# Kernel tuning notes

Measured on AMD Instinct MI355X. Metric: run time of the kernel, lower is better.

Reference implementation:

```python
import jax, jax.numpy as jnp
import numpy as np

D = 4096       # hidden_size
H = 32         # n_heads (tp_size=1)
DN = 128       # qk_nope_head_dim
DR = 64        # qk_rope_head_dim
DV = 128       # v_head_dim
QL = 1536      # q_lora_rank
KL = 512       # kv_lora_rank
S = 2048       # seqlen, start_pos = 0
EPS = 1e-6
SCALE = (DN + DR) ** -0.5  # softmax_scale (no yarn mscale: seqlen <= original_seq_len)
THETA = 10000.0


def _freqs(seqlen, dim, base=THETA):
    # precompute_freqs_cis without yarn correction (seqlen <= original_seq_len)
    inv = 1.0 / (base ** (np.arange(0, dim, 2, dtype=np.float32) / dim))
    f = np.outer(np.arange(seqlen, dtype=np.float32), inv)  # [S, dim//2]
    return jnp.asarray(np.cos(f)), jnp.asarray(np.sin(f))


def _rmsnorm(x, w):
    return x * jax.lax.rsqrt(jnp.mean(x * x, axis=-1, keepdims=True) + EPS) * w


def _rope(x, cos, sin):
    # x: [S, H, R]; complex rotation on consecutive pairs (view_as_complex semantics)
    S_, H_, R_ = x.shape
    xr = x.reshape(S_, H_, R_ // 2, 2)
    x0, x1 = xr[..., 0], xr[..., 1]
    c = cos[:, None, :]
    s = sin[:, None, :]
    y0 = x0 * c - x1 * s
    y1 = x0 * s + x1 * c
    return jnp.stack([y0, y1], axis=-1).reshape(S_, H_, R_)


def setup_inputs() -> dict:
    key = jax.random.key(0)
    ks = jax.random.split(key, 6)
    std = 0.02
    return {
        "x": jax.random.normal(ks[0], (S, D), jnp.float32),
        "wq_a": jax.random.normal(ks[1], (QL, D), jnp.float32) * std,
        "q_norm_w": jnp.ones((QL,), jnp.float32),
        "wq_b": jax.random.normal(ks[2], (H * (DN + DR), QL), jnp.float32) * std,
        "wkv_a": jax.random.normal(ks[3], (KL + DR, D), jnp.float32) * std,
        "kv_norm_w": jnp.ones((KL,), jnp.float32),
        "wkv_b": jax.random.normal(ks[4], (H * (DN + DV), KL), jnp.float32) * std,
        "wo": jax.random.normal(ks[5], (D, H * DV), jnp.float32) * std,
    }


def reference(x, wq_a, q_norm_w, wq_b, wkv_a, kv_norm_w, wkv_b, wo):
    cos, sin = _freqs(S, DR)

    # q path: low-rank down-proj + RMSNorm + up-proj
    q = _rmsnorm(x @ wq_a.T, q_norm_w) @ wq_b.T          # [S, H*(DN+DR)]
    q = q.reshape(S, H, DN + DR)
    q_nope, q_pe = q[..., :DN], q[..., DN:]
    q_pe = _rope(q_pe, cos, sin)                          # [S, H, DR]

    # kv path: joint latent + rope part
    kv_all = x @ wkv_a.T                                  # [S, KL+DR]
    kv = _rmsnorm(kv_all[:, :KL], kv_norm_w)              # latent kv cache [S, KL]
    k_pe = _rope(kv_all[:, None, KL:], cos, sin)[:, 0, :]  # pe cache [S, DR]

    # absorb k-up-projection into q (einsum 'shd,hdc->shc')
    wkv_b_r = wkv_b.reshape(H, DN + DV, KL)
    q_lat = jnp.einsum("shd,hdc->shc", q_nope, wkv_b_r[:, :DN])  # [S, H, KL]

    scores = (jnp.einsum("shc,tc->sht", q_lat, kv)
              + jnp.einsum("shr,tr->sht", q_pe, k_pe)) * SCALE   # [S, H, T]

    causal = jnp.arange(S)[:, None] >= jnp.arange(S)[None, :]     # [S, T]
    scores = jnp.where(causal[:, None, :], scores, -jnp.inf)
    p = jax.nn.softmax(scores, axis=-1)

    o_lat = jnp.einsum("sht,tc->shc", p, kv)                      # [S, H, KL]
    o = jnp.einsum("shc,hdc->shd", o_lat, wkv_b_r[:, DN:])        # [S, H, DV]
    return o.reshape(S, H * DV) @ wo.T                            # [S, D]
```

## Files before the change

### kernel.cpp

```cpp
#include <hip/hip_runtime.h>
#include <hip/hip_bf16.h>
#include <type_traits>

using bf16 = __hip_bfloat16;
typedef short v8s __attribute__((ext_vector_type(8)));
typedef float v4f __attribute__((ext_vector_type(4)));

#define DEV __device__ __forceinline__

constexpr float SCALE_ = 0.07216878364870322f;

DEV unsigned short bfu(float f) {
  bf16 h = __float2bfloat16(f);
  return __builtin_bit_cast(unsigned short, h);
}
DEV float b2f(short u) {
  unsigned int x = ((unsigned int)(unsigned short)u) << 16;
  return __builtin_bit_cast(float, x);
}

DEV void g2lds16(const void* g, void* l) {
  __builtin_amdgcn_global_load_lds(
      (const __attribute__((address_space(1))) unsigned int*)g,
      (__attribute__((address_space(3))) unsigned int*)l, 16, 0, 0);
}


__global__ void cast_kernel(const float* __restrict__ in, bf16* __restrict__ out, int n4) {
  int i = blockIdx.x * 256 + threadIdx.x;
  int stride = gridDim.x * 256;
  for (; i < n4; i += stride) {
    float4 v = ((const float4*)in)[i];
    ushort4 u;
    u.x = bfu(v.x); u.y = bfu(v.y); u.z = bfu(v.z); u.w = bfu(v.w);
    ((ushort4*)out)[i] = u;
  }
}

__global__ void cast_pad_kernel(const float* __restrict__ in, bf16* __restrict__ out) {
  int i = blockIdx.x * 256 + threadIdx.x;
  float4 v = make_float4(0.f, 0.f, 0.f, 0.f);
  if (i < 589824) v = ((const float4*)in)[i];
  ushort4 u;
  u.x = bfu(v.x); u.y = bfu(v.y); u.z = bfu(v.z); u.w = bfu(v.w);
  ((ushort4*)out)[i] = u;
}

__global__ void wkvbt_kernel(const float* __restrict__ wkvb, bf16* __restrict__ out) {
  int gid = blockIdx.x * 256 + threadIdx.x;
  int c8 = (gid & 63) * 8;
  int d8 = ((gid >> 6) & 15) * 8;
  int h = gid >> 10;
  float4 a[8][2];
#pragma unroll
  for (int r = 0; r < 8; ++r) {
    const float* p = wkvb + ((long)(h * 256 + d8 + r)) * 512 + c8;
    a[r][0] = *(const float4*)p;
    a[r][1] = *(const float4*)(p + 4);
  }
#pragma unroll
  for (int cc = 0; cc < 8; ++cc) {
    v8s o;
#pragma unroll
    for (int r = 0; r < 8; ++r) {
      float f = (cc < 4) ? ((const float*)&a[r][0])[cc] : ((const float*)&a[r][1])[cc - 4];
      o[r] = (short)bfu(f);
    }
    *(v8s*)(out + (long)h * 65536 + (c8 + cc) * 128 + d8) = o;
  }
}

__global__ void wkvbv_kernel(const float* __restrict__ wkvb, bf16* __restrict__ out) {
  int i = blockIdx.x * 256 + threadIdx.x;
  int c4 = i & 127, d = (i >> 7) & 127, h = i >> 14;
  float4 v = *(const float4*)(wkvb + ((long)(h * 256 + 128 + d)) * 512 + c4 * 4);
  ushort4 u;
  u.x = bfu(v.x); u.y = bfu(v.y); u.z = bfu(v.z); u.w = bfu(v.w);
  *(ushort4*)(out + ((long)(h * 128 + d)) * 512 + c4 * 4) = u;
}

__global__ void freqs_kernel(float* __restrict__ cosb, float* __restrict__ sinb) {
  int t = blockIdx.x * 256 + threadIdx.x;
  int s = t >> 5, i = t & 31;
  float inv = powf(10000.0f, -(float)(2 * i) / 64.0f);
  float f = (float)s * inv;
  cosb[t] = cosf(f);
  sinb[t] = sinf(f);
}

__global__ void rmsnorm_bf_kernel(const bf16* __restrict__ in, const float* __restrict__ w,
                                  bf16* __restrict__ out, int L, int ldin, int ldout) {
  int row = blockIdx.x;
  const bf16* x = in + (long)row * ldin;
  int L8 = L >> 3;
  float ss = 0.f;
  for (int i = threadIdx.x; i < L8; i += 256) {
    v8s v = *(const v8s*)(x + i * 8);
#pragma unroll
    for (int j = 0; j < 8; ++j) { float f = b2f(v[j]); ss += f * f; }
  }
#pragma unroll
  for (int d = 1; d < 64; d <<= 1) ss += __shfl_xor(ss, d);
  __shared__ float red[4];
  if ((threadIdx.x & 63) == 0) red[threadIdx.x >> 6] = ss;
  __syncthreads();
  float r = rsqrtf((red[0] + red[1] + red[2] + red[3]) / (float)L + 1e-6f);
  bf16* o = out + (long)row * ldout;
  for (int i = threadIdx.x; i < L8; i += 256) {
    v8s v = *(const v8s*)(x + i * 8);
    v8s u;
#pragma unroll
    for (int j = 0; j < 8; ++j)
      u[j] = (short)bfu(b2f(v[j]) * r * w[i * 8 + j]);
    *(v8s*)(o + i * 8) = u;
  }
}

__global__ void rope_kpe_kernel(const bf16* __restrict__ qakv, const float* __restrict__ cosb,
                                const float* __restrict__ sinb, bf16* __restrict__ keff) {
  int t = blockIdx.x * 256 + threadIdx.x;
  int s = t >> 5, i = t & 31;
  const bf16* p = qakv + (long)s * 2176 + 2048;
  float x0 = __bfloat162float(p[2 * i]), x1 = __bfloat162float(p[2 * i + 1]);
  float c = cosb[t], sn = sinb[t];
  bf16* o = keff + (long)s * 576 + 512;
  o[2 * i] = __float2bfloat16(x0 * c - x1 * sn);
  o[2 * i + 1] = __float2bfloat16(x0 * sn + x1 * c);
}

__global__ void rope_q_kernel(const bf16* __restrict__ qf, const float* __restrict__ cosb,
                              const float* __restrict__ sinb, bf16* __restrict__ qeff) {
  int t = blockIdx.x * 256 + threadIdx.x;
  int i = t & 31, h = (t >> 5) & 31, s = t >> 10;
  const bf16* p = qf + (long)s * 6144 + h * 192 + 128;
  float x0 = __bfloat162float(p[2 * i]), x1 = __bfloat162float(p[2 * i + 1]);
  float c = cosb[s * 32 + i], sn = sinb[s * 32 + i];
  bf16* o = qeff + (long)s * 18432 + h * 576 + 512;
  o[2 * i] = __float2bfloat16(x0 * c - x1 * sn);
  o[2 * i + 1] = __float2bfloat16(x0 * sn + x1 * c);
}

__global__ void vtrans_kernel(const bf16* __restrict__ keff, bf16* __restrict__ vT) {
  int gid = blockIdx.x * 256 + threadIdx.x;
  int t8 = (gid & 255) * 8, c8 = (gid >> 8) * 8;
  v8s in[8];
#pragma unroll
  for (int r = 0; r < 8; ++r)
    in[r] = *(const v8s*)(keff + (long)(t8 + r) * 576 + c8);
#pragma unroll
  for (int cc = 0; cc < 8; ++cc) {
    v8s o;
#pragma unroll
    for (int r = 0; r < 8; ++r) o[r] = in[r][cc];
    *(v8s*)(vT + (long)(c8 + cc) * 2048 + t8) = o;
  }
}

template <typename OutT>
__global__ __launch_bounds__(256, 3) void gemm_bt(
    const bf16* __restrict__ A, const bf16* __restrict__ B, OutT* __restrict__ C,
    int K, int lda, int ldb, int ldc, long sA, long sB, long sC) {
  __shared__ bf16 lA[4096];
  __shared__ bf16 lB[4096];
  const int tid = threadIdx.x;
  const int lane = tid & 63;
  const int w = tid >> 6, wm = w >> 1, wn = w & 1;
  const int r16 = lane & 15, kg = (lane >> 4) << 3;
  const int arow = tid >> 2, acol = (tid & 3) << 3;
  const bf16* Ab = A + (long)blockIdx.z * sA + (long)blockIdx.y * 128 * lda;
  const bf16* Bb = B + (long)blockIdx.z * sB + (long)blockIdx.x * 128 * ldb;
  v4f acc[4][4] = {};
  for (int k0 = 0; k0 < K; k0 += 32) {
    __syncthreads();
#pragma unroll
    for (int i = 0; i < 2; ++i) {
      g2lds16(Ab + (long)(i * 64 + arow) * lda + (k0 + acol), &lA[i * 2048 + w * 512]);
      g2lds16(Bb + (long)(i * 64 + arow) * ldb + (k0 + acol), &lB[i * 2048 + w * 512]);
    }
    __syncthreads();
    v8s af[4], bfr[4];
#pragma unroll
    for (int mi = 0; mi < 4; ++mi)
      af[mi] = *(const v8s*)&lA[(wm * 64 + mi * 16 + r16) * 32 + kg];
#pragma unroll
    for (int ni = 0; ni < 4; ++ni)
      bfr[ni] = *(const v8s*)&lB[(wn * 64 + ni * 16 + r16) * 32 + kg];
    __builtin_amdgcn_s_setprio(1);
#pragma unroll
    for (int mi = 0; mi < 4; ++mi)
#pragma unroll
      for (int ni = 0; ni < 4; ++ni)
        acc[mi][ni] = __builtin_amdgcn_mfma_f32_16x16x32_bf16(af[mi], bfr[ni], acc[mi][ni], 0, 0, 0);
    __builtin_amdgcn_s_setprio(0);
  }
  OutT* Cb = C + (long)blockIdx.z * sC + (long)(blockIdx.y * 128) * ldc + blockIdx.x * 128;
  const int cr = (lane >> 4) << 2;
#pragma unroll
  for (int mi = 0; mi < 4; ++mi)
#pragma unroll
    for (int ni = 0; ni < 4; ++ni)
#pragma unroll
      for (int j = 0; j < 4; ++j) {
        long idx = (long)(wm * 64 + mi * 16 + cr + j) * ldc + wn * 64 + ni * 16 + r16;
        float v = acc[mi][ni][j];
        if constexpr (std::is_same<OutT, float>::value) Cb[idx] = v;
        else Cb[idx] = __float2bfloat16(v);
      }
}

__global__ __launch_bounds__(256, 2) void gemm_k128(
    const bf16* __restrict__ A, const bf16* __restrict__ B, bf16* __restrict__ C,
    int lda, int ldb, int ldc, long sA, long sB, long sC) {
  __shared__ bf16 lA[16384];
  __shared__ bf16 lB[16384];
  const int tid = threadIdx.x;
  const int lane = tid & 63;
  const int w = tid >> 6, wm = w >> 1, wn = w & 1;
  const int r16 = lane & 15, hi = lane >> 4;
  const bf16* Ab = A + (long)blockIdx.z * sA + (long)blockIdx.y * 128 * lda;
  const bf16* Bb = B + (long)blockIdx.z * sB + (long)blockIdx.x * 128 * ldb;
#pragma unroll
  for (int it = 0; it < 8; ++it) {
    int D = it * 256 + tid;
    int row = D >> 4, sl = D & 15;
    int gs = sl ^ (row & 7);
    g2lds16(Ab + (long)row * lda + gs * 8, (char*)lA + (it * 256 + w * 64) * 16);
    g2lds16(Bb + (long)row * ldb + gs * 8, (char*)lB + (it * 256 + w * 64) * 16);
  }
  __syncthreads();
  v4f acc[4][4] = {};
#pragma unroll
  for (int kk = 0; kk < 4; ++kk) {
    v8s af[4], bfr[4];
#pragma unroll
    for (int mi = 0; mi < 4; ++mi) {
      int r = wm * 64 + mi * 16 + r16;
      af[mi] = *(const v8s*)((const char*)lA + (r * 16 + ((kk * 4 + hi) ^ (r & 7))) * 16);
    }
#pragma unroll
    for (int ni = 0; ni < 4; ++ni) {
      int r = wn * 64 + ni * 16 + r16;
      bfr[ni] = *(const v8s*)((const char*)lB + (r * 16 + ((kk * 4 + hi) ^ (r & 7))) * 16);
    }
    __builtin_amdgcn_s_setprio(1);
#pragma unroll
    for (int mi = 0; mi < 4; ++mi)
#pragma unroll
      for (int ni = 0; ni < 4; ++ni)
        acc[mi][ni] = __builtin_amdgcn_mfma_f32_16x16x32_bf16(af[mi], bfr[ni], acc[mi][ni], 0, 0, 0);
    __builtin_amdgcn_s_setprio(0);
  }
  bf16* Cb = C + (long)blockIdx.z * sC + (long)(blockIdx.y * 128) * ldc + blockIdx.x * 128;
  const int cr = hi << 2;
#pragma unroll
  for (int mi = 0; mi < 4; ++mi)
#pragma unroll
    for (int ni = 0; ni < 4; ++ni)
#pragma unroll
      for (int j = 0; j < 4; ++j) {
        long idx = (long)(wm * 64 + mi * 16 + cr + j) * ldc + wn * 64 + ni * 16 + r16;
        Cb[idx] = __float2bfloat16(acc[mi][ni][j]);
      }
}

__device__ const signed char U_QT[24] = {15,15,7,14,14,13,13,6,12,12,11,11,5,10,10,9,9,4,8,8,3,2,1,0};
__device__ const signed char U_HF[24] = {0,1,-1,0,1,0,1,-1,0,1,0,1,-1,0,1,0,1,-1,0,1,-1,-1,-1,-1};

__global__ __launch_bounds__(512, 2) void attn_kernel(
    const bf16* __restrict__ qeff, const bf16* __restrict__ keff,
    const bf16* __restrict__ vT, bf16* __restrict__ olat,
    bf16* __restrict__ P1, float* __restrict__ mlb) {
  __shared__ __align__(16) bf16 kl[32 * 576];
  __shared__ __align__(16) bf16 vl[512 * 32];
  const int tid = threadIdx.x, lane = tid & 63, w = tid >> 6;
  const int r16 = lane & 15, hi = lane >> 4;
  const int kg = hi << 3, cr = hi << 2;
  const int h = blockIdx.x;
  const int u = blockIdx.y;
  const int qt = U_QT[u];
  const int hf = U_HF[u];
  const int nch = 4 * qt + 4;
  const int kc0 = (hf == 1) ? (nch >> 1) : 0;
  const int kc1 = (hf == 0) ? (nch >> 1) : nch;
  const int qrow = qt * 128 + w * 16 + r16;
  const int rb = r16 & 7;

  const long qbase = (long)qrow * 18432 + h * 576;
  v8s qreg[18];
#pragma unroll
  for (int kk = 0; kk < 18; ++kk)
    qreg[kk] = __builtin_nontemporal_load((const v8s*)(qeff + qbase + kk * 32 + kg));

  v4f acc[32] = {};
  float mrow = -1e30f, lrow = 0.f;

  auto stageK = [&](int t0) {
#pragma unroll
    for (int it = 0; it < 5; ++it) {
      int D = it * 512 + tid;
      if (D < 2304) {
        int row = D / 72;
        int gg = D - row * 72;
        int gs = gg ^ (row & 7);
        g2lds16(keff + (long)(t0 + row) * 576 + gs * 8,
                (char*)kl + (it * 512 + w * 64) * 16);
      }
    }
  };
  auto stageV = [&](int t0) {
#pragma unroll
    for (int it = 0; it < 4; ++it) {
      int D = it * 512 + tid;
      int row = D >> 2;
      int s = (D & 3) ^ ((row >> 1) & 3);
      g2lds16(vT + (long)row * 2048 + t0 + s * 8,
              (char*)vl + (it * 512 + w * 64) * 16);
    }
  };

  stageK(kc0 * 32);
  __syncthreads();

  for (int kc = kc0; kc < kc1; ++kc) {
    const int t0 = kc * 32;
    stageV(t0);

    const char* kb = (const char*)kl;
    v4f sf0 = {}, sf1 = {};
    __builtin_amdgcn_s_setprio(1);
#pragma unroll
    for (int kk = 0; kk < 18; ++kk) {
      int so = ((kk * 4 + hi) ^ rb) << 4;
      v8s b0 = *(const v8s*)(kb + r16 * 1152 + so);
      v8s b1 = *(const v8s*)(kb + (16 + r16) * 1152 + so);
      sf0 = __builtin_amdgcn_mfma_f32_16x16x32_bf16(b0, qreg[kk], sf0, 0, 0, 0);
      sf1 = __builtin_amdgcn_mfma_f32_16x16x32_bf16(b1, qreg[kk], sf1, 0, 0, 0);
    }
    __builtin_amdgcn_s_setprio(0);
    float s0[4], s1[4];
#pragma unroll
    for (int j = 0; j < 4; ++j) { s0[j] = sf0[j] * SCALE_; s1[j] = sf1[j] * SCALE_; }
    if (kc >= 4 * qt) {
#pragma unroll
      for (int j = 0; j < 4; ++j) {
        if (t0 + cr + j > qrow) s0[j] = -1e30f;
        if (t0 + 16 + cr + j > qrow) s1[j] = -1e30f;
      }
    }
    float mx = fmaxf(fmaxf(fmaxf(s0[0], s0[1]), fmaxf(s0[2], s0[3])),
                     fmaxf(fmaxf(s1[0], s1[1]), fmaxf(s1[2], s1[3])));
    mx = fmaxf(mx, __shfl_xor(mx, 16));
    mx = fmaxf(mx, __shfl_xor(mx, 32));
    if (!__all(mx <= mrow + 8.0f)) {
      float mn = fmaxf(mrow, mx);
      float alpha = __expf(mrow - mn);
      mrow = mn;
      lrow *= alpha;
      float af0 = __shfl(alpha, cr + 0), af1 = __shfl(alpha, cr + 1);
      float af2 = __shfl(alpha, cr + 2), af3 = __shfl(alpha, cr + 3);
#pragma unroll
      for (int c = 0; c < 32; ++c) {
        acc[c][0] *= af0; acc[c][1] *= af1; acc[c][2] *= af2; acc[c][3] *= af3;
      }
    }
    float p0[4], p1[4];
#pragma unroll
    for (int j = 0; j < 4; ++j) {
      p0[j] = __expf(s0[j] - mrow);
      p1[j] = __expf(s1[j] - mrow);
    }
    float rs = (p0[0] + p0[1]) + (p0[2] + p0[3]) + (p1[0] + p1[1]) + (p1[2] + p1[3]);
    rs += __shfl_xor(rs, 16);
    rs += __shfl_xor(rs, 32);
    lrow += rs;
    int u0 = (int)((unsigned)bfu(p0[0]) | ((unsigned)bfu(p0[1]) << 16));
    int u1 = (int)((unsigned)bfu(p0[2]) | ((unsigned)bfu(p0[3]) << 16));
    int v0 = (int)((unsigned)bfu(p1[0]) | ((unsigned)bfu(p1[1]) << 16));
    int v1 = (int)((unsigned)bfu(p1[2]) | ((unsigned)bfu(p1[3]) << 16));
    const int L1 = r16 + 32 * (hi & 1);
    const int L2 = L1 + 16;
    const bool lo = hi < 2;
    int d0a = __shfl(u0, L1), d0b = __shfl(v0, L1);
    int d1a = __shfl(u1, L1), d1b = __shfl(v1, L1);
    int d2a = __shfl(u0, L2), d2b = __shfl(v0, L2);
    int d3a = __shfl(u1, L2), d3b = __shfl(v1, L2);
    int4 pw = make_int4(lo ? d0a : d0b, lo ? d1a : d1b, lo ? d2a : d2b, lo ? d3a : d3b);
    v8s ap = __builtin_bit_cast(v8s, pw);

    __syncthreads();
    if (kc + 1 < kc1) stageK(t0 + 32);

    __builtin_amdgcn_s_setprio(1);
#pragma unroll
    for (int c = 0; c < 32; ++c) {
      const int vrow = c * 16 + r16;
      const int vsw = (hi ^ ((vrow >> 1) & 3)) << 4;
      v8s bv = *(const v8s*)((const char*)vl + vrow * 64 + vsw);
      acc[c] = __builtin_amdgcn_mfma_f32_16x16x32_bf16(ap, bv, acc[c], 0, 0, 0);
    }
    __builtin_amdgcn_s_setprio(0);
    __syncthreads();
  }
  if (hf < 0) {
    float linv0 = 1.0f / __shfl(lrow, cr + 0);
    float linv1 = 1.0f / __shfl(lrow, cr + 1);
    float linv2 = 1.0f / __shfl(lrow, cr + 2);
    float linv3 = 1.0f / __shfl(lrow, cr + 3);
    const long ob = (long)(qt * 128 + w * 16 + cr) * 16384 + h * 512 + r16;
#pragma unroll
    for (int c = 0; c < 32; ++c) {
      olat[ob + 0 * 16384 + c * 16] = __float2bfloat16(acc[c][0] * linv0);
      olat[ob + 1 * 16384 + c * 16] = __float2bfloat16(acc[c][1] * linv1);
      olat[ob + 2 * 16384 + c * 16] = __float2bfloat16(acc[c][2] * linv2);
      olat[ob + 3 * 16384 + c * 16] = __float2bfloat16(acc[c][3] * linv3);
    }
  } else {
    if (hi == 0) {
      float* mr = mlb + (((qrow - 1024) << 5) + h) * 4 + hf * 2;
      mr[0] = mrow;
      mr[1] = lrow;
    }
    bf16* dst = (hf == 0) ? olat : P1;
    const int rbase = (hf == 0) ? (qt * 128) : (qt * 128 - 1024);
    const long ob = (long)(rbase + w * 16 + cr) * 16384 + h * 512 + r16;
#pragma unroll
    for (int c = 0; c < 32; ++c) {
      dst[ob + 0 * 16384 + c * 16] = __float2bfloat16(acc[c][0]);
      dst[ob + 1 * 16384 + c * 16] = __float2bfloat16(acc[c][1]);
      dst[ob + 2 * 16384 + c * 16] = __float2bfloat16(acc[c][2]);
      dst[ob + 3 * 16384 + c * 16] = __float2bfloat16(acc[c][3]);
    }
  }
}

__global__ void combine_kernel(bf16* __restrict__ olat, const bf16* __restrict__ P1,
                               const float* __restrict__ mlb) {
  int gid = blockIdx.x * 256 + threadIdx.x;
  int cg = gid & 63, h = (gid >> 6) & 31, r = gid >> 11;
  const float* m4 = mlb + ((r << 5) + h) * 4;
  float mA = m4[0], lA = m4[1], mB = m4[2], lB = m4[3];
  float m = fmaxf(mA, mB);
  float sA = __expf(mA - m), sB = __expf(mB - m);
  float inv = 1.0f / (sA * lA + sB * lB);
  sA *= inv; sB *= inv;
  long oa = (long)(1024 + r) * 16384 + h * 512 + cg * 8;
  long ob = (long)r * 16384 + h * 512 + cg * 8;
  v8s a = *(const v8s*)(olat + oa);
  v8s b = *(const v8s*)(P1 + ob);
  v8s o;
#pragma unroll
  for (int j = 0; j < 8; ++j)
    o[j] = (short)bfu(b2f(a[j]) * sA + b2f(b[j]) * sB);
  *(v8s*)(olat + oa) = o;
}


extern "C" void kernel_launch(void* const* d_in, const int* in_sizes, int n_in,
                              void* d_out, int out_size, void* d_ws, size_t ws_size,
                              hipStream_t stream) {
  const float* x = (const float*)d_in[0];
  const float* wq_a = (const float*)d_in[1];
  const float* q_norm_w = (const float*)d_in[2];
  const float* wq_b = (const float*)d_in[3];
  const float* wkv_a = (const float*)d_in[4];
  const float* kv_norm_w = (const float*)d_in[5];
  const float* wkv_b = (const float*)d_in[6];
  const float* wo = (const float*)d_in[7];
  char* ws = (char*)d_ws;

  float* cosb  = (float*)(ws + 0);
  float* sinb  = (float*)(ws + 262144);
  bf16* qeffb  = (bf16*)(ws + 524288);
  bf16* olat   = (bf16*)(ws + 76021760);
  bf16* keff   = (bf16*)(ws + 143130624);
  bf16* vTb    = (bf16*)(ws + 145489920);
  bf16* P1b    = (bf16*)(ws + 147587072);
  float* mlb   = (float*)(ws + 181141504);
  bf16* xb     = (bf16*)(ws + 76021760);
  bf16* wqab   = (bf16*)(ws + 92798976);
  bf16* wkvabp = (bf16*)(ws + 105381888);
  bf16* qakv   = (bf16*)(ws + 110624768);
  bf16* qan    = (bf16*)(ws + 125829120);
  bf16* wqbb   = (bf16*)(ws + 76021760);
  bf16* qf     = (bf16*)(ws + 94896128);
  bf16* wkvb1t = (bf16*)(ws + 76021760);
  bf16* wkvbv  = (bf16*)(ws + 524288);
  bf16* obuf   = (bf16*)(ws + 4718592);
  bf16* wob    = (bf16*)(ws + 21495808);

  cast_kernel<<<2048, 256, 0, stream>>>(x, xb, 2097152);
  cast_kernel<<<2048, 256, 0, stream>>>(wq_a, wqab, 1572864);
  cast_pad_kernel<<<2560, 256, 0, stream>>>(wkv_a, wkvabp);
  freqs_kernel<<<256, 256, 0, stream>>>(cosb, sinb);

  gemm_bt<bf16><<<dim3(17, 16, 1), 256, 0, stream>>>(xb, wqab, qakv, 4096, 4096, 4096, 2176, 0, 0, 0);

  rmsnorm_bf_kernel<<<2048, 256, 0, stream>>>(qakv, q_norm_w, qan, 1536, 2176, 1536);
  rmsnorm_bf_kernel<<<2048, 256, 0, stream>>>(qakv + 1536, kv_norm_w, keff, 512, 2176, 576);
  rope_kpe_kernel<<<256, 256, 0, stream>>>(qakv, cosb, sinb, keff);
  vtrans_kernel<<<64, 256, 0, stream>>>(keff, vTb);

  cast_kernel<<<2048, 256, 0, stream>>>(wq_b, wqbb, 2359296);
  gemm_bt<bf16><<<dim3(48, 16, 1), 256, 0, stream>>>(qan, wqbb, qf, 1536, 1536, 1536, 6144, 0, 0, 0);

  rope_q_kernel<<<8192, 256, 0, stream>>>(qf, cosb, sinb, qeffb);
  wkvbt_kernel<<<128, 256, 0, stream>>>(wkv_b, wkvb1t);
  gemm_k128<<<dim3(4, 16, 32), 256, 0, stream>>>(qf, wkvb1t, qeffb,
      6144, 128, 18432, 192L, 65536L, 576L);

  attn_kernel<<<dim3(32, 24), 512, 0, stream>>>(qeffb, keff, vTb, olat, P1b, mlb);
  combine_kernel<<<8192, 256, 0, stream>>>(olat, P1b, mlb);

  wkvbv_kernel<<<2048, 256, 0, stream>>>(wkv_b, wkvbv);
  gemm_bt<bf16><<<dim3(1, 16, 32), 256, 0, stream>>>(olat, wkvbv, obuf,
      512, 16384, 512, 4096, 512L, 65536L, 128L);

  cast_kernel<<<2048, 256, 0, stream>>>(wo, wob, 4194304);
  gemm_bt<float><<<dim3(32, 16, 1), 256, 0, stream>>>(obuf, wob, (float*)d_out,
      4096, 4096, 4096, 4096, 0, 0, 0);
}
```

Measured before the change: 645.6 us.

## Repartition PV accumulation so each wave owns a latent-column slice across all query rows

The P·V stage is re-split across waves. Previously each wave held its 16 query rows against all 512 latent columns and read every V fragment from LDS. Now each wave holds all 128 query rows against a 64-column slice: it loads only four V fragments and reads the P tiles and rescale factors that every wave writes to new shared buffers. This cuts redundant V reads from LDS and removes the cross-lane shuffles used to build the P operand. In exchange it adds LDS writes and reads for P and alpha, applies the rescale on every chunk instead of only when the max changes, and needs an extra barrier before the epilogue.

Measured after the change: 716.9 us. +11.0%, slower.

```diff
diff --git a/kernel.cpp b/kernel.cpp
--- a/kernel.cpp
+++ b/kernel.cpp
@@ -272,6 +272,8 @@
     bf16* __restrict__ P1, float* __restrict__ mlb) {
   __shared__ __align__(16) bf16 kl[32 * 576];
   __shared__ __align__(16) bf16 vl[512 * 32];
+  __shared__ __align__(16) bf16 pl[128 * 40];
+  __shared__ __align__(16) float alf[128];
   const int tid = threadIdx.x, lane = tid & 63, w = tid >> 6;
   const int r16 = lane & 15, hi = lane >> 4;
   const int kg = hi << 3, cr = hi << 2;
@@ -351,17 +353,12 @@
                      fmaxf(fmaxf(s1[0], s1[1]), fmaxf(s1[2], s1[3])));
     mx = fmaxf(mx, __shfl_xor(mx, 16));
     mx = fmaxf(mx, __shfl_xor(mx, 32));
+    float alpha = 1.0f;
     if (!__all(mx <= mrow + 8.0f)) {
       float mn = fmaxf(mrow, mx);
-      float alpha = __expf(mrow - mn);
+      alpha = __expf(mrow - mn);
       mrow = mn;
       lrow *= alpha;
-      float af0 = __shfl(alpha, cr + 0), af1 = __shfl(alpha, cr + 1);
-      float af2 = __shfl(alpha, cr + 2), af3 = __shfl(alpha, cr + 3);
-#pragma unroll
-      for (int c = 0; c < 32; ++c) {
-        acc[c][0] *= af0; acc[c][1] *= af1; acc[c][2] *= af2; acc[c][3] *= af3;
-      }
     }
     float p0[4], p1[4];
 #pragma unroll
@@ -373,63 +370,80 @@
     rs += __shfl_xor(rs, 16);
     rs += __shfl_xor(rs, 32);
     lrow += rs;
-    int u0 = (int)((unsigned)bfu(p0[0]) | ((unsigned)bfu(p0[1]) << 16));
-    int u1 = (int)((unsigned)bfu(p0[2]) | ((unsigned)bfu(p0[3]) << 16));
-    int v0 = (int)((unsigned)bfu(p1[0]) | ((unsigned)bfu(p1[1]) << 16));
-    int v1 = (int)((unsigned)bfu(p1[2]) | ((unsigned)bfu(p1[3]) << 16));
-    const int L1 = r16 + 32 * (hi & 1);
-    const int L2 = L1 + 16;
-    const bool lo = hi < 2;
-    int d0a = __shfl(u0, L1), d0b = __shfl(v0, L1);
-    int d1a = __shfl(u1, L1), d1b = __shfl(v1, L1);
-    int d2a = __shfl(u0, L2), d2b = __shfl(v0, L2);
-    int d3a = __shfl(u1, L2), d3b = __shfl(v1, L2);
-    int4 pw = make_int4(lo ? d0a : d0b, lo ? d1a : d1b, lo ? d2a : d2b, lo ? d3a : d3b);
-    v8s ap = __builtin_bit_cast(v8s, pw);
+    {
+      int u0 = (int)((unsigned)bfu(p0[0]) | ((unsigned)bfu(p0[1]) << 16));
+      int u1 = (int)((unsigned)bfu(p0[2]) | ((unsigned)bfu(p0[3]) << 16));
+      int v0 = (int)((unsigned)bfu(p1[0]) | ((unsigned)bfu(p1[1]) << 16));
+      int v1 = (int)((unsigned)bfu(p1[2]) | ((unsigned)bfu(p1[3]) << 16));
+      const int q = w * 16 + r16;
+      char* prow = (char*)pl + q * 80;
+      *(int2*)(prow + hi * 8) = make_int2(u0, u1);
+      *(int2*)(prow + 32 + hi * 8) = make_int2(v0, v1);
+      if (hi == 0) alf[q] = alpha;
+    }
 
     __syncthreads();
     if (kc + 1 < kc1) stageK(t0 + 32);
 
+    v8s bv[4];
+#pragma unroll
+    for (int cfc = 0; cfc < 4; ++cfc) {
+      const int vrow = w * 64 + cfc * 16 + r16;
+      const int vsw = (hi ^ ((vrow >> 1) & 3)) << 4;
+      bv[cfc] = *(const v8s*)((const char*)vl + vrow * 64 + vsw);
+    }
     __builtin_amdgcn_s_setprio(1);
 #pragma unroll
-    for (int c = 0; c < 32; ++c) {
-      const int vrow = c * 16 + r16;
-      const int vsw = (hi ^ ((vrow >> 1) & 3)) << 4;
-      v8s bv = *(const v8s*)((const char*)vl + vrow * 64 + vsw);
-      acc[c] = __builtin_amdgcn_mfma_f32_16x16x32_bf16(ap, bv, acc[c], 0, 0, 0);
+    for (int qb = 0; qb < 8; ++qb) {
+      v8s pa = *(const v8s*)((const char*)pl + (qb * 16 + r16) * 80 + hi * 16);
+      v4f af4 = *(const v4f*)&alf[qb * 16 + (hi << 2)];
+#pragma unroll
+      for (int cfc = 0; cfc < 4; ++cfc) {
+        v4f a = acc[qb * 4 + cfc];
+        a[0] *= af4[0]; a[1] *= af4[1]; a[2] *= af4[2]; a[3] *= af4[3];
+        acc[qb * 4 + cfc] = __builtin_amdgcn_mfma_f32_16x16x32_bf16(pa, bv[cfc], a, 0, 0, 0);
+      }
     }
     __builtin_amdgcn_s_setprio(0);
     __syncthreads();
   }
+  if (hf >= 0 && hi == 0) {
+    float* mr = mlb + (((qrow - 1024) << 5) + h) * 4 + hf * 2;
+    mr[0] = mrow;
+    mr[1] = lrow;
+  }
+  if (hi == 0) alf[w * 16 + r16] = lrow;
+  __syncthreads();
   if (hf < 0) {
-    float linv0 = 1.0f / __shfl(lrow, cr + 0);
-    float linv1 = 1.0f / __shfl(lrow, cr + 1);
-    float linv2 = 1.0f / __shfl(lrow, cr + 2);
-    float linv3 = 1.0f / __shfl(lrow, cr + 3);
-    const long ob = (long)(qt * 128 + w * 16 + cr) * 16384 + h * 512 + r16;
-#pragma unroll
-    for (int c = 0; c < 32; ++c) {
-      olat[ob + 0 * 16384 + c * 16] = __float2bfloat16(acc[c][0] * linv0);
-      olat[ob + 1 * 16384 + c * 16] = __float2bfloat16(acc[c][1] * linv1);
-      olat[ob + 2 * 16384 + c * 16] = __float2bfloat16(acc[c][2] * linv2);
-      olat[ob + 3 * 16384 + c * 16] = __float2bfloat16(acc[c][3] * linv3);
+#pragma unroll
+    for (int qb = 0; qb < 8; ++qb) {
+      v4f lf4 = *(const v4f*)&alf[qb * 16 + (hi << 2)];
+      float linv0 = 1.0f / lf4[0], linv1 = 1.0f / lf4[1];
+      float linv2 = 1.0f / lf4[2], linv3 = 1.0f / lf4[3];
+#pragma unroll
+      for (int cfc = 0; cfc < 4; ++cfc) {
+        const long base = (long)(qt * 128 + qb * 16 + (hi << 2)) * 16384 + h * 512 + w * 64 + cfc * 16 + r16;
+        v4f a = acc[qb * 4 + cfc];
+        olat[base + 0 * 16384] = __float2bfloat16(a[0] * linv0);
+        olat[base + 1 * 16384] = __float2bfloat16(a[1] * linv1);
+        olat[base + 2 * 16384] = __float2bfloat16(a[2] * linv2);
+        olat[base + 3 * 16384] = __float2bfloat16(a[3] * linv3);
+      }
     }
   } else {
-    if (hi == 0) {
-      float* mr = mlb + (((qrow - 1024) << 5) + h) * 4 + hf * 2;
-      mr[0] = mrow;
-      mr[1] = lrow;
-    }
     bf16* dst = (hf == 0) ? olat : P1;
     const int rbase = (hf == 0) ? (qt * 128) : (qt * 128 - 1024);
-    const long ob = (long)(rbase + w * 16 + cr) * 16384 + h * 512 + r16;
-#pragma unroll
-    for (int c = 0; c < 32; ++c) {
-      dst[ob + 0 * 16384 + c * 16] = __float2bfloat16(acc[c][0]);
-      dst[ob + 1 * 16384 + c * 16] = __float2bfloat16(acc[c][1]);
-      dst[ob + 2 * 16384 + c * 16] = __float2bfloat16(acc[c][2]);
-      dst[ob + 3 * 16384 + c * 16] = __float2bfloat16(acc[c][3]);
-    }
+#pragma unroll
+    for (int qb = 0; qb < 8; ++qb)
+#pragma unroll
+      for (int cfc = 0; cfc < 4; ++cfc) {
+        const long base = (long)(rbase + qb * 16 + (hi << 2)) * 16384 + h * 512 + w * 64 + cfc * 16 + r16;
+        v4f a = acc[qb * 4 + cfc];
+        dst[base + 0 * 16384] = __float2bfloat16(a[0]);
+        dst[base + 1 * 16384] = __float2bfloat16(a[1]);
+        dst[base + 2 * 16384] = __float2bfloat16(a[2]);
+        dst[base + 3 * 16384] = __float2bfloat16(a[3]);
+      }
   }
 }
 
```
